# Kernel optimization log

Measured on AMD Instinct MI355X. Metric: run time of the kernel, lower is better.

## Reference

```python
import jax, jax.numpy as jnp
import numpy as np
import math

D_MODEL = 1024
NUM_HEADS = 16
HEAD_DIM = D_MODEL // NUM_HEADS


def setup_inputs() -> dict:
    key = jax.random.key(0)
    ks = jax.random.split(key, 8)
    B, S, D = 8, 1024, D_MODEL
    scale = 1.0 / math.sqrt(D)
    return {
        "x": jax.random.normal(ks[0], (B, S, D), dtype=jnp.float32),
        "Wq": jax.random.normal(ks[1], (D, D), dtype=jnp.float32) * scale,
        "bq": jax.random.normal(ks[2], (D,), dtype=jnp.float32) * 0.02,
        "Wk": jax.random.normal(ks[3], (D, D), dtype=jnp.float32) * scale,
        "bk": jax.random.normal(ks[4], (D,), dtype=jnp.float32) * 0.02,
        "Wv": jax.random.normal(ks[5], (D, D), dtype=jnp.float32) * scale,
        "bv": jax.random.normal(ks[6], (D,), dtype=jnp.float32) * 0.02,
        "structure_bias": jax.random.normal(ks[7], (NUM_HEADS, 1, 1), dtype=jnp.float32),
    }


def reference(x, Wq, bq, Wk, bk, Wv, bv, structure_bias):
    # x: [B, S, D]; Linear weights in torch layout [out, in]: y = x @ W.T + b
    B, S, D = x.shape
    H, Dh = NUM_HEADS, HEAD_DIM

    def proj(W, b):
        # [B, S, D] -> [B, H, S, Dh]
        y = jnp.einsum('bsd,ed->bse', x, W) + b
        return y.reshape(B, S, H, Dh).transpose(0, 2, 1, 3)

    Q = proj(Wq, bq)
    K = proj(Wk, bk)
    V = proj(Wv, bv)

    # scores: [B, H, S, S] with per-head scalar bias broadcast
    scores = jnp.einsum('bhqd,bhkd->bhqk', Q, K) / math.sqrt(Dh)
    scores = scores + structure_bias  # [H,1,1] broadcasts over [B,H,S,S]
    attention = jax.nn.softmax(scores, axis=-1)
    # dropout(p=0.1) is identity in eval mode
    context = jnp.einsum('bhqk,bhkd->bhqd', attention, V)
    context = context.transpose(0, 2, 1, 3).reshape(B, S, D)
    return (context, attention)
```

## Files before the change

### kernel.cpp

```cpp
#include <hip/hip_runtime.h>
#include <cstdint>
#include <cstddef>


typedef _Float16 f16;
typedef __attribute__((__ext_vector_type__(8))) _Float16 f16x8;
typedef __attribute__((__ext_vector_type__(4))) _Float16 f16x4;
typedef __attribute__((__ext_vector_type__(4))) float fx4;

#define GLL16(g, l)                                                         \
  __builtin_amdgcn_global_load_lds(                                         \
      (const __attribute__((address_space(1))) void*)(g),                   \
      (__attribute__((address_space(3))) void*)(l), 16, 0, 0)
#define WAIT_VM0() asm volatile("s_waitcnt vmcnt(0)" ::: "memory")
#define WAIT_LGKM0() asm volatile("s_waitcnt lgkmcnt(0)" ::: "memory")

__global__ __launch_bounds__(256) void cvt_x(const float* __restrict__ src,
                                             f16* __restrict__ dst) {
  int i = blockIdx.x * 256 + threadIdx.x;
  float4 v = ((const float4*)src)[i];
  f16x4 o = {(f16)v.x, (f16)v.y, (f16)v.z, (f16)v.w};
  *(f16x4*)(dst + (size_t)i * 4) = o;
}

__global__ __launch_bounds__(256) void cvt_w(const float* __restrict__ wq,
                                             const float* __restrict__ wk,
                                             const float* __restrict__ wv,
                                             f16* __restrict__ dst) {
  int z = blockIdx.y;
  const float* s = (z == 0) ? wq : ((z == 1) ? wk : wv);
  int i = blockIdx.x * 256 + threadIdx.x;
  float4 v = ((const float4*)s)[i];
  f16x4 o = {(f16)v.x, (f16)v.y, (f16)v.z, (f16)v.w};
  *(f16x4*)(dst + (size_t)z * 1048576 + (size_t)i * 4) = o;
}

__global__ __launch_bounds__(256) void proj_kernel(
    const f16* __restrict__ xb, const f16* __restrict__ Wb,
    const float* __restrict__ bq, const float* __restrict__ bk,
    const float* __restrict__ bv, f16* __restrict__ Qb, f16* __restrict__ Kb,
    f16* __restrict__ Vt) {
  const int t = threadIdx.x;
  const int lane = t & 63, wid = t >> 6;
  const int r16 = lane & 15, quad = lane >> 4;
  const int wm = wid >> 1, wn = wid & 1;
  const int n0 = blockIdx.x * 128, m0 = blockIdx.y * 128, z = blockIdx.z;
  __shared__ f16 As[4096];
  __shared__ f16 Bs[4096];
  const f16* Wz = Wb + (size_t)z * 1048576;
  const int lrow = t >> 2, lcol = (t & 3) * 8;
  const f16* Ag = xb + (size_t)(m0 + lrow) * 1024 + lcol;
  const f16* Bg = Wz + (size_t)(n0 + lrow) * 1024 + lcol;
  f16* Al = As + t * 8;
  f16* Bl = Bs + t * 8;

  fx4 acc[4][4];
  const fx4 z4 = {0.f, 0.f, 0.f, 0.f};
#pragma unroll
  for (int i = 0; i < 4; ++i)
#pragma unroll
    for (int j = 0; j < 4; ++j) acc[i][j] = z4;

  for (int kt = 0; kt < 32; ++kt) {
    const int k0 = kt * 32;
    GLL16(Ag + k0, Al);
    GLL16(Ag + k0 + 65536, Al + 2048);
    GLL16(Bg + k0, Bl);
    GLL16(Bg + k0 + 65536, Bl + 2048);
    WAIT_VM0();
    __syncthreads();
    f16x8 a[4], bfr[4];
#pragma unroll
    for (int mi = 0; mi < 4; ++mi)
      a[mi] = *(const f16x8*)(As + (wm * 64 + mi * 16 + r16) * 32 + quad * 8);
#pragma unroll
    for (int ni = 0; ni < 4; ++ni)
      bfr[ni] = *(const f16x8*)(Bs + (wn * 64 + ni * 16 + r16) * 32 + quad * 8);
#pragma unroll
    for (int mi = 0; mi < 4; ++mi)
#pragma unroll
      for (int ni = 0; ni < 4; ++ni)
        acc[mi][ni] = __builtin_amdgcn_mfma_f32_16x16x32_f16(
            a[mi], bfr[ni], acc[mi][ni], 0, 0, 0);
    __syncthreads();
  }

  const float* bias = (z == 0) ? bq : ((z == 1) ? bk : bv);
  float bvals[4];
#pragma unroll
  for (int ni = 0; ni < 4; ++ni) bvals[ni] = bias[n0 + wn * 64 + ni * 16 + r16];

#pragma unroll
  for (int mi = 0; mi < 4; ++mi) {
#pragma unroll
    for (int ni = 0; ni < 4; ++ni) {
      const int gn = n0 + wn * 64 + ni * 16 + r16;
      const int hh = gn >> 6, dh = gn & 63;
#pragma unroll
      for (int r = 0; r < 4; ++r) {
        const int gm = m0 + wm * 64 + mi * 16 + quad * 4 + r;
        const int bi = gm >> 10, s = gm & 1023;
        float v = acc[mi][ni][r] + bvals[ni];
        if (z == 0) {
          Qb[((size_t)((bi * 16 + hh) * 1024 + s)) * 64 + dh] =
              (f16)(v * 0.125f);
        } else if (z == 1) {
          Kb[((size_t)((bi * 16 + hh) * 1024 + s)) * 64 + dh] = (f16)v;
        } else {
          Vt[((size_t)((bi * 16 + hh) * 64 + dh)) * 1024 + s] = (f16)v;
        }
      }
    }
  }
}

__global__ __launch_bounds__(256) void attn_kernel(
    const f16* __restrict__ Qb, const f16* __restrict__ Kb,
    const f16* __restrict__ Vt, float* __restrict__ ctx,
    float* __restrict__ attn) {
  const int t = threadIdx.x;
  const int lane = t & 63, w = t >> 6;
  const int r16 = lane & 15, quad = lane >> 4;
  const int qt = blockIdx.x, h = blockIdx.y, b = blockIdx.z;
  __shared__ f16 Qs[4096];
  __shared__ f16 Ks[4096];
  __shared__ f16 Vs[4096];
  __shared__ f16 Ps[4096];
  const size_t bh = (size_t)(b * 16 + h);
  const f16* Qg = Qb + (bh * 1024 + (size_t)qt * 64) * 64;
  const f16* Kh = Kb + bh * 65536;
  const f16* Vh = Vt + bh * 65536;
  float* attnB = attn + bh * 1048576 + (size_t)(qt * 64) * 1024;

  const int lrow = t >> 2, lc8 = (t & 3) * 8;
  const int qkoff = lrow * 64 + lc8;
  const int voff = lrow * 1024 + lc8;
  f16* Ql = Qs + t * 8;
  f16* Kl = Ks + t * 8;
  f16* Vl = Vs + t * 8;

  GLL16(Qg + qkoff, Ql);
  GLL16(Qg + qkoff + 32, Ql + 2048);
  GLL16(Kh + qkoff, Kl);
  GLL16(Kh + qkoff + 32, Kl + 2048);
  WAIT_VM0();
  __syncthreads();

  const f16x8 aq0 = *(const f16x8*)(Qs + (w * 16 + r16) * 32 + quad * 8);
  const f16x8 aq1 = *(const f16x8*)(Qs + 2048 + (w * 16 + r16) * 32 + quad * 8);

  const fx4 z4 = {0.f, 0.f, 0.f, 0.f};
  float m_[4], lp[4];
#pragma unroll
  for (int r = 0; r < 4; ++r) {
    m_[r] = -1e30f;
    lp[r] = 0.f;
  }

  for (int kt = 0; kt < 16; ++kt) {
    f16x8 bk[4][2];
#pragma unroll
    for (int ni = 0; ni < 4; ++ni) {
      bk[ni][0] = *(const f16x8*)(Ks + (ni * 16 + r16) * 32 + quad * 8);
      bk[ni][1] = *(const f16x8*)(Ks + 2048 + (ni * 16 + r16) * 32 + quad * 8);
    }
    fx4 s[4];
#pragma unroll
    for (int ni = 0; ni < 4; ++ni) {
      s[ni] = __builtin_amdgcn_mfma_f32_16x16x32_f16(aq0, bk[ni][0], z4, 0, 0, 0);
      s[ni] = __builtin_amdgcn_mfma_f32_16x16x32_f16(aq1, bk[ni][1], s[ni], 0, 0, 0);
    }
    __syncthreads();
    if (kt < 15) {
      const f16* Kg = Kh + (size_t)(kt + 1) * 4096;
      GLL16(Kg + qkoff, Kl);
      GLL16(Kg + qkoff + 32, Kl + 2048);
    } else {
      GLL16(Kh + qkoff, Kl);
      GLL16(Kh + qkoff + 32, Kl + 2048);
      GLL16(Vh + voff, Vl);
      GLL16(Vh + voff + 32, Vl + 2048);
    }
#pragma unroll
    for (int ri = 0; ri < 4; ++ri) {
      float rm = fmaxf(fmaxf(s[0][ri], s[1][ri]), fmaxf(s[2][ri], s[3][ri]));
      rm = fmaxf(rm, __shfl_xor(rm, 1));
      rm = fmaxf(rm, __shfl_xor(rm, 2));
      rm = fmaxf(rm, __shfl_xor(rm, 4));
      rm = fmaxf(rm, __shfl_xor(rm, 8));
      const float mn = fmaxf(m_[ri], rm);
      const float corr = __expf(m_[ri] - mn);
      const float ps = __expf(s[0][ri] - mn) + __expf(s[1][ri] - mn) +
                       __expf(s[2][ri] - mn) + __expf(s[3][ri] - mn);
      lp[ri] = lp[ri] * corr + ps;
      m_[ri] = mn;
    }
    WAIT_VM0();
    __syncthreads();
  }

  float inv_l[4];
#pragma unroll
  for (int ri = 0; ri < 4; ++ri) {
    float ls = lp[ri];
    ls += __shfl_xor(ls, 1);
    ls += __shfl_xor(ls, 2);
    ls += __shfl_xor(ls, 4);
    ls += __shfl_xor(ls, 8);
    inv_l[ri] = 1.0f / ls;
  }

  fx4 o[4];
#pragma unroll
  for (int ni = 0; ni < 4; ++ni) o[ni] = z4;

  for (int kt = 0; kt < 16; ++kt) {
    f16x8 bk[4][2], bv[4][2];
#pragma unroll
    for (int ni = 0; ni < 4; ++ni) {
      bk[ni][0] = *(const f16x8*)(Ks + (ni * 16 + r16) * 32 + quad * 8);
      bk[ni][1] = *(const f16x8*)(Ks + 2048 + (ni * 16 + r16) * 32 + quad * 8);
      bv[ni][0] = *(const f16x8*)(Vs + (ni * 16 + r16) * 32 + quad * 8);
      bv[ni][1] = *(const f16x8*)(Vs + 2048 + (ni * 16 + r16) * 32 + quad * 8);
    }
    fx4 s[4];
#pragma unroll
    for (int ni = 0; ni < 4; ++ni) {
      s[ni] = __builtin_amdgcn_mfma_f32_16x16x32_f16(aq0, bk[ni][0], z4, 0, 0, 0);
      s[ni] = __builtin_amdgcn_mfma_f32_16x16x32_f16(aq1, bk[ni][1], s[ni], 0, 0, 0);
    }
    __syncthreads();
    if (kt < 15) {
      const f16* Kg = Kh + (size_t)(kt + 1) * 4096;
      GLL16(Kg + qkoff, Kl);
      GLL16(Kg + qkoff + 32, Kl + 2048);
      GLL16(Vh + voff + (kt + 1) * 64, Vl);
      GLL16(Vh + voff + (kt + 1) * 64 + 32, Vl + 2048);
    }
#pragma unroll
    for (int ni = 0; ni < 4; ++ni) {
#pragma unroll
      for (int ri = 0; ri < 4; ++ri) {
        const float p = __expf(s[ni][ri] - m_[ri]) * inv_l[ri];
        attnB[(size_t)(w * 16 + quad * 4 + ri) * 1024 + kt * 64 + ni * 16 +
              r16] = p;
        Ps[(ni >> 1) * 2048 + (w * 16 + quad * 4 + ri) * 32 + (ni & 1) * 16 +
           r16] = (f16)p;
      }
    }
    WAIT_LGKM0();
    const f16x8 ap0 = *(const f16x8*)(Ps + (w * 16 + r16) * 32 + quad * 8);
    const f16x8 ap1 = *(const f16x8*)(Ps + 2048 + (w * 16 + r16) * 32 + quad * 8);
#pragma unroll
    for (int ni = 0; ni < 4; ++ni) {
      o[ni] = __builtin_amdgcn_mfma_f32_16x16x32_f16(ap0, bv[ni][0], o[ni], 0, 0, 0);
      o[ni] = __builtin_amdgcn_mfma_f32_16x16x32_f16(ap1, bv[ni][1], o[ni], 0, 0, 0);
    }
    WAIT_VM0();
    __syncthreads();
  }

  float* ctxB = ctx + ((size_t)b * 1024 + (size_t)qt * 64) * 1024 + h * 64;
#pragma unroll
  for (int ni = 0; ni < 4; ++ni)
#pragma unroll
    for (int ri = 0; ri < 4; ++ri)
      ctxB[(size_t)(w * 16 + quad * 4 + ri) * 1024 + ni * 16 + r16] =
          o[ni][ri];
}

extern "C" void kernel_launch(void* const* d_in, const int* in_sizes, int n_in,
                              void* d_out, int out_size, void* d_ws,
                              size_t ws_size, hipStream_t stream) {
  const float* x = (const float*)d_in[0];
  const float* Wq = (const float*)d_in[1];
  const float* bq = (const float*)d_in[2];
  const float* Wk = (const float*)d_in[3];
  const float* bk = (const float*)d_in[4];
  const float* Wv = (const float*)d_in[5];
  const float* bv = (const float*)d_in[6];

  char* ws = (char*)d_ws;
  f16* xb = (f16*)(ws);
  f16* Wb = (f16*)(ws + (16u << 20));
  f16* Qb = (f16*)(ws + (22u << 20));
  f16* Kb = (f16*)(ws + (38u << 20));
  f16* Vt = (f16*)(ws + (54u << 20));

  float* ctx = (float*)d_out;
  float* attn = (float*)d_out + 8388608;

  cvt_x<<<dim3(8192), dim3(256), 0, stream>>>(x, xb);
  cvt_w<<<dim3(1024, 3), dim3(256), 0, stream>>>(Wq, Wk, Wv, Wb);
  proj_kernel<<<dim3(8, 64, 3), dim3(256), 0, stream>>>(xb, Wb, bq, bk, bv, Qb,
                                                        Kb, Vt);
  attn_kernel<<<dim3(16, 16, 8), dim3(256), 0, stream>>>(Qb, Kb, Vt, ctx, attn);
}
```

Baseline: 810.6 us.

## Double-buffer K/V tiles, drop online max, load Q directly into registers

Double-buffers the K and V shared-memory tiles so the next tile's global-to-LDS load is issued before computing on the current one, with one barrier per iteration instead of two. It removes the running-max tracking in the first pass and exponentiates raw scores, which relies on scores being small enough not to overflow. Q fragments are now read straight from global memory into registers, and the second pass uses a partial vmcnt wait so the attn stores need not drain before the barrier. The partial wait count and the dropped max subtraction add risk around load completion and numerical safety.

```diff
diff --git a/kernel.cpp b/kernel.cpp
--- a/kernel.cpp
+++ b/kernel.cpp
@@ -13,7 +13,10 @@
       (const __attribute__((address_space(1))) void*)(g),                   \
       (__attribute__((address_space(3))) void*)(l), 16, 0, 0)
 #define WAIT_VM0() asm volatile("s_waitcnt vmcnt(0)" ::: "memory")
+#define WAIT_VM12() asm volatile("s_waitcnt vmcnt(12)" ::: "memory")
 #define WAIT_LGKM0() asm volatile("s_waitcnt lgkmcnt(0)" ::: "memory")
+#define SBAR() __builtin_amdgcn_s_barrier()
+#define SCHED_PIN() __builtin_amdgcn_sched_barrier(0)
 
 __global__ __launch_bounds__(256) void cvt_x(const float* __restrict__ src,
                                              f16* __restrict__ dst) {
@@ -122,9 +125,8 @@
   const int lane = t & 63, w = t >> 6;
   const int r16 = lane & 15, quad = lane >> 4;
   const int qt = blockIdx.x, h = blockIdx.y, b = blockIdx.z;
-  __shared__ f16 Qs[4096];
-  __shared__ f16 Ks[4096];
-  __shared__ f16 Vs[4096];
+  __shared__ f16 Ks[2][4096];
+  __shared__ f16 Vs[2][4096];
   __shared__ f16 Ps[4096];
   const size_t bh = (size_t)(b * 16 + h);
   const f16* Qg = Qb + (bh * 1024 + (size_t)qt * 64) * 64;
@@ -135,68 +137,51 @@
   const int lrow = t >> 2, lc8 = (t & 3) * 8;
   const int qkoff = lrow * 64 + lc8;
   const int voff = lrow * 1024 + lc8;
-  f16* Ql = Qs + t * 8;
-  f16* Kl = Ks + t * 8;
-  f16* Vl = Vs + t * 8;
-
-  GLL16(Qg + qkoff, Ql);
-  GLL16(Qg + qkoff + 32, Ql + 2048);
-  GLL16(Kh + qkoff, Kl);
-  GLL16(Kh + qkoff + 32, Kl + 2048);
+
+  const f16* qrow = Qg + (w * 16 + r16) * 64 + quad * 8;
+  const f16x8 aq0 = *(const f16x8*)(qrow);
+  const f16x8 aq1 = *(const f16x8*)(qrow + 32);
+
+  GLL16(Kh + qkoff, &Ks[0][0] + t * 8);
+  GLL16(Kh + qkoff + 32, &Ks[0][0] + t * 8 + 2048);
   WAIT_VM0();
-  __syncthreads();
-
-  const f16x8 aq0 = *(const f16x8*)(Qs + (w * 16 + r16) * 32 + quad * 8);
-  const f16x8 aq1 = *(const f16x8*)(Qs + 2048 + (w * 16 + r16) * 32 + quad * 8);
+  SBAR();
 
   const fx4 z4 = {0.f, 0.f, 0.f, 0.f};
-  float m_[4], lp[4];
-#pragma unroll
-  for (int r = 0; r < 4; ++r) {
-    m_[r] = -1e30f;
-    lp[r] = 0.f;
-  }
+  float lp[4] = {0.f, 0.f, 0.f, 0.f};
 
   for (int kt = 0; kt < 16; ++kt) {
-    f16x8 bk[4][2];
-#pragma unroll
-    for (int ni = 0; ni < 4; ++ni) {
-      bk[ni][0] = *(const f16x8*)(Ks + (ni * 16 + r16) * 32 + quad * 8);
-      bk[ni][1] = *(const f16x8*)(Ks + 2048 + (ni * 16 + r16) * 32 + quad * 8);
-    }
-    fx4 s[4];
-#pragma unroll
-    for (int ni = 0; ni < 4; ++ni) {
-      s[ni] = __builtin_amdgcn_mfma_f32_16x16x32_f16(aq0, bk[ni][0], z4, 0, 0, 0);
-      s[ni] = __builtin_amdgcn_mfma_f32_16x16x32_f16(aq1, bk[ni][1], s[ni], 0, 0, 0);
-    }
-    __syncthreads();
+    const int cb = kt & 1, nb = cb ^ 1;
     if (kt < 15) {
       const f16* Kg = Kh + (size_t)(kt + 1) * 4096;
-      GLL16(Kg + qkoff, Kl);
-      GLL16(Kg + qkoff + 32, Kl + 2048);
+      GLL16(Kg + qkoff, &Ks[nb][0] + t * 8);
+      GLL16(Kg + qkoff + 32, &Ks[nb][0] + t * 8 + 2048);
     } else {
-      GLL16(Kh + qkoff, Kl);
-      GLL16(Kh + qkoff + 32, Kl + 2048);
-      GLL16(Vh + voff, Vl);
-      GLL16(Vh + voff + 32, Vl + 2048);
-    }
-#pragma unroll
-    for (int ri = 0; ri < 4; ++ri) {
-      float rm = fmaxf(fmaxf(s[0][ri], s[1][ri]), fmaxf(s[2][ri], s[3][ri]));
-      rm = fmaxf(rm, __shfl_xor(rm, 1));
-      rm = fmaxf(rm, __shfl_xor(rm, 2));
-      rm = fmaxf(rm, __shfl_xor(rm, 4));
-      rm = fmaxf(rm, __shfl_xor(rm, 8));
-      const float mn = fmaxf(m_[ri], rm);
-      const float corr = __expf(m_[ri] - mn);
-      const float ps = __expf(s[0][ri] - mn) + __expf(s[1][ri] - mn) +
-                       __expf(s[2][ri] - mn) + __expf(s[3][ri] - mn);
-      lp[ri] = lp[ri] * corr + ps;
-      m_[ri] = mn;
-    }
+      GLL16(Kh + qkoff, &Ks[0][0] + t * 8);
+      GLL16(Kh + qkoff + 32, &Ks[0][0] + t * 8 + 2048);
+      GLL16(Vh + voff, &Vs[0][0] + t * 8);
+      GLL16(Vh + voff + 32, &Vs[0][0] + t * 8 + 2048);
+    }
+    f16x8 bk0[4], bk1[4];
+#pragma unroll
+    for (int ni = 0; ni < 4; ++ni) {
+      bk0[ni] = *(const f16x8*)(&Ks[cb][0] + (ni * 16 + r16) * 32 + quad * 8);
+      bk1[ni] =
+          *(const f16x8*)(&Ks[cb][0] + 2048 + (ni * 16 + r16) * 32 + quad * 8);
+    }
+    fx4 s[4];
+#pragma unroll
+    for (int ni = 0; ni < 4; ++ni) {
+      s[ni] = __builtin_amdgcn_mfma_f32_16x16x32_f16(aq0, bk0[ni], z4, 0, 0, 0);
+      s[ni] =
+          __builtin_amdgcn_mfma_f32_16x16x32_f16(aq1, bk1[ni], s[ni], 0, 0, 0);
+    }
+#pragma unroll
+    for (int ri = 0; ri < 4; ++ri)
+      lp[ri] += __expf(s[0][ri]) + __expf(s[1][ri]) + __expf(s[2][ri]) +
+                __expf(s[3][ri]);
     WAIT_VM0();
-    __syncthreads();
+    SBAR();
   }
 
   float inv_l[4];
@@ -215,49 +200,60 @@
   for (int ni = 0; ni < 4; ++ni) o[ni] = z4;
 
   for (int kt = 0; kt < 16; ++kt) {
-    f16x8 bk[4][2], bv[4][2];
-#pragma unroll
-    for (int ni = 0; ni < 4; ++ni) {
-      bk[ni][0] = *(const f16x8*)(Ks + (ni * 16 + r16) * 32 + quad * 8);
-      bk[ni][1] = *(const f16x8*)(Ks + 2048 + (ni * 16 + r16) * 32 + quad * 8);
-      bv[ni][0] = *(const f16x8*)(Vs + (ni * 16 + r16) * 32 + quad * 8);
-      bv[ni][1] = *(const f16x8*)(Vs + 2048 + (ni * 16 + r16) * 32 + quad * 8);
-    }
-    fx4 s[4];
-#pragma unroll
-    for (int ni = 0; ni < 4; ++ni) {
-      s[ni] = __builtin_amdgcn_mfma_f32_16x16x32_f16(aq0, bk[ni][0], z4, 0, 0, 0);
-      s[ni] = __builtin_amdgcn_mfma_f32_16x16x32_f16(aq1, bk[ni][1], s[ni], 0, 0, 0);
-    }
-    __syncthreads();
+    const int cb = kt & 1, nb = cb ^ 1;
     if (kt < 15) {
       const f16* Kg = Kh + (size_t)(kt + 1) * 4096;
-      GLL16(Kg + qkoff, Kl);
-      GLL16(Kg + qkoff + 32, Kl + 2048);
-      GLL16(Vh + voff + (kt + 1) * 64, Vl);
-      GLL16(Vh + voff + (kt + 1) * 64 + 32, Vl + 2048);
+      GLL16(Kg + qkoff, &Ks[nb][0] + t * 8);
+      GLL16(Kg + qkoff + 32, &Ks[nb][0] + t * 8 + 2048);
+      GLL16(Vh + voff + (kt + 1) * 64, &Vs[nb][0] + t * 8);
+      GLL16(Vh + voff + (kt + 1) * 64 + 32, &Vs[nb][0] + t * 8 + 2048);
+    }
+    SCHED_PIN();
+    f16x8 bk0[4], bk1[4];
+#pragma unroll
+    for (int ni = 0; ni < 4; ++ni) {
+      bk0[ni] = *(const f16x8*)(&Ks[cb][0] + (ni * 16 + r16) * 32 + quad * 8);
+      bk1[ni] =
+          *(const f16x8*)(&Ks[cb][0] + 2048 + (ni * 16 + r16) * 32 + quad * 8);
+    }
+    fx4 s[4];
+#pragma unroll
+    for (int ni = 0; ni < 4; ++ni) {
+      s[ni] = __builtin_amdgcn_mfma_f32_16x16x32_f16(aq0, bk0[ni], z4, 0, 0, 0);
+      s[ni] =
+          __builtin_amdgcn_mfma_f32_16x16x32_f16(aq1, bk1[ni], s[ni], 0, 0, 0);
     }
 #pragma unroll
     for (int ni = 0; ni < 4; ++ni) {
 #pragma unroll
       for (int ri = 0; ri < 4; ++ri) {
-        const float p = __expf(s[ni][ri] - m_[ri]) * inv_l[ri];
+        const float p = __expf(s[ni][ri]) * inv_l[ri];
         attnB[(size_t)(w * 16 + quad * 4 + ri) * 1024 + kt * 64 + ni * 16 +
               r16] = p;
         Ps[(ni >> 1) * 2048 + (w * 16 + quad * 4 + ri) * 32 + (ni & 1) * 16 +
            r16] = (f16)p;
       }
     }
+    f16x8 bv0[4], bv1[4];
+#pragma unroll
+    for (int ni = 0; ni < 4; ++ni) {
+      bv0[ni] = *(const f16x8*)(&Vs[cb][0] + (ni * 16 + r16) * 32 + quad * 8);
+      bv1[ni] =
+          *(const f16x8*)(&Vs[cb][0] + 2048 + (ni * 16 + r16) * 32 + quad * 8);
+    }
     WAIT_LGKM0();
     const f16x8 ap0 = *(const f16x8*)(Ps + (w * 16 + r16) * 32 + quad * 8);
-    const f16x8 ap1 = *(const f16x8*)(Ps + 2048 + (w * 16 + r16) * 32 + quad * 8);
-#pragma unroll
-    for (int ni = 0; ni < 4; ++ni) {
-      o[ni] = __builtin_amdgcn_mfma_f32_16x16x32_f16(ap0, bv[ni][0], o[ni], 0, 0, 0);
-      o[ni] = __builtin_amdgcn_mfma_f32_16x16x32_f16(ap1, bv[ni][1], o[ni], 0, 0, 0);
-    }
-    WAIT_VM0();
-    __syncthreads();
+    const f16x8 ap1 =
+        *(const f16x8*)(Ps + 2048 + (w * 16 + r16) * 32 + quad * 8);
+#pragma unroll
+    for (int ni = 0; ni < 4; ++ni) {
+      o[ni] =
+          __builtin_amdgcn_mfma_f32_16x16x32_f16(ap0, bv0[ni], o[ni], 0, 0, 0);
+      o[ni] =
+          __builtin_amdgcn_mfma_f32_16x16x32_f16(ap1, bv1[ni], o[ni], 0, 0, 0);
+    }
+    WAIT_VM12();
+    SBAR();
   }
 
   float* ctxB = ctx + ((size_t)b * 1024 + (size_t)qt * 64) * 1024 + h * 64;
```

Measured after the change: 797.6 us. No clear change (-1.6%).
